# Kernel optimization log

Hardware: AMD Instinct MI355X
Metric: run time of the kernel (lower is better)

The kernel has to match this reference:

```python
import jax, jax.numpy as jnp
import numpy as np

LR = 0.1          # learning_rate
THRESHOLD = 0.1   # surprise_threshold (fixed; adaptive_threshold=False / eval path)
TEMP = 0.1        # temperature
EPS = 1e-6

B, S, DK, DV = 64, 1024, 128, 128


def setup_inputs() -> dict:
    key = jax.random.key(0)
    k1, k2 = jax.random.split(key)
    return {
        "memory": jnp.zeros((B, DV, DK), dtype=jnp.float32),
        "key": jax.random.normal(k1, (B, S, DK), dtype=jnp.float32),
        "value": jax.random.normal(k2, (B, S, DV), dtype=jnp.float32),
    }


def reference(memory, key, value):
    # memory: (B, DV, DK); key: (B, S, DK); value: (B, S, DV)
    # Sequential delta-rule fast-weight update with surprise gating.
    def step(mem, kv):
        k_t, v_t = kv                                  # (B, DK), (B, DV)
        k_n = k_t / (jnp.linalg.norm(k_t, axis=-1, keepdims=True) + EPS)
        predicted = jnp.einsum('bvk,bk->bv', mem, k_n)  # (B, DV)
        surprise = predicted - v_t                      # (B, DV)
        s_norm = jnp.linalg.norm(surprise, axis=-1, keepdims=True)  # (B, 1)
        gate = jax.nn.sigmoid((s_norm - THRESHOLD) / TEMP)          # (B, 1)
        # forget_term + lr*learn_term = (predicted + lr*surprise) outer k_n
        update = (predicted + LR * surprise)[:, :, None] * k_n[:, None, :]
        mem = mem - gate[:, :, None] * update
        return mem, gate

    # scan over the sequence axis
    kv_seq = (jnp.swapaxes(key, 0, 1), jnp.swapaxes(value, 0, 1))  # (S, B, *)
    mem_final, gates = jax.lax.scan(step, memory, kv_seq)
    gate_values = jnp.swapaxes(gates, 0, 1)  # (B, S, 1)
    return mem_final, gate_values
```

## Files before the change

### kernel.cpp

```cpp
#include <hip/hip_runtime.h>
#include <math.h>

#define B_    64
#define S_    1024
#define DK_   128
#define DV_   128
#define T_    16
#define NC_   (S_ / T_)
#define KP_   (DK_ + 4)
#define LR_   0.1f
#define LRP1_ 1.1f
#define THR_  0.1f
#define ITEMP_ 10.0f
#define EPS_  1e-6f

template<int CTRL>
__device__ __forceinline__ float dpp_add(float x) {
  int t = __builtin_amdgcn_update_dpp(0, __float_as_int(x), CTRL, 0xf, 0xf, true);
  return x + __int_as_float(t);
}
__device__ __forceinline__ float wave_sum64(float x) {
  x = dpp_add<0x111>(x); x = dpp_add<0x112>(x); x = dpp_add<0x114>(x);
  x = dpp_add<0x118>(x); x = dpp_add<0x142>(x); x = dpp_add<0x143>(x);
  return __int_as_float(__builtin_amdgcn_readlane(__float_as_int(x), 63));
}
__device__ __forceinline__ float row16_sum(float x) {
  x = dpp_add<0x111>(x); x = dpp_add<0x112>(x);
  x = dpp_add<0x114>(x); x = dpp_add<0x118>(x);
  return x;
}
__device__ __forceinline__ float rdlane(float v, int l) {
  return __int_as_float(__builtin_amdgcn_readlane(__float_as_int(v), l));
}
__device__ __forceinline__ float dot4(float4 a, float4 b) {
  return fmaf(a.x, b.x, fmaf(a.y, b.y, fmaf(a.z, b.z, a.w * b.w)));
}
__device__ __forceinline__ void gll16(const float* g, float* l) {
  __builtin_amdgcn_global_load_lds(
      (const __attribute__((address_space(1))) unsigned int*)g,
      (__attribute__((address_space(3))) unsigned int*)l, 16, 0, 0);
}

__global__ __launch_bounds__(512, 2)
void sgm_kernel(const float* __restrict__ mem_in,
                const float* __restrict__ key,
                const float* __restrict__ value,
                float* __restrict__ out) {
  const int b = blockIdx.x, tid = threadIdx.x;
  const int g = tid >> 4, h = tid & 15, lane = tid & 63, wv = tid >> 6;

  __shared__ __align__(16) float kS[2][T_][KP_];
  __shared__ __align__(16) float vS[2][T_][KP_];
  __shared__ __align__(16) float rawL[T_][DK_];
  __shared__ __align__(16) float cuL[T_][DK_];
  __shared__ __align__(16) float GT[2][T_][T_];
  __shared__ __align__(16) float gateL[S_];

  float4 mA[4], mB[4];
  {
    const float4* Mp = reinterpret_cast<const float4*>(mem_in + (size_t)b * DV_ * DK_);
    #pragma unroll
    for (int rr = 0; rr < 4; ++rr) {
      mA[rr] = Mp[(4*g + rr) * 32 + h];
      mB[rr] = Mp[(4*g + rr) * 32 + 16 + h];
    }
  }
  const float* kb = key   + (size_t)b * S_ * DK_;
  const float* vb = value + (size_t)b * S_ * DV_;

  const int pPair = (tid - 64) >> 1;
  int tP = 0, jP = 0;
  {
    int t = 0, pp = pPair;
    if (wv > 0 && pPair < 136) {
      while (pp > t) { pp -= (t + 1); ++t; }
      tP = t; jP = pp;
    }
  }

  auto stage = [&](int cc) {
    if (wv == 0 && lane < 32) {
      #pragma unroll
      for (int t = 0; t < T_; ++t)
        gll16(kb + (size_t)(cc*T_ + t)*DK_ + lane*4, &kS[cc & 1][t][0]);
    }
    if (wv == 1 && lane < 32) {
      #pragma unroll
      for (int t = 0; t < T_; ++t)
        gll16(vb + (size_t)(cc*T_ + t)*DV_ + lane*4, &vS[cc & 1][t][0]);
    }
  };

  float4 kxR[16];

  auto applyUpdate = [&](int pb) {
    #pragma unroll
    for (int j = 0; j < T_; ++j) {
      const float4* kj = reinterpret_cast<const float4*>(&kS[pb][j][0]);
      const float4 ky = kj[16 + h];
      const float4 cu = *reinterpret_cast<const float4*>(&cuL[j][4 * g]);
      const float cc4[4] = {cu.x, cu.y, cu.z, cu.w};
      #pragma unroll
      for (int rr = 0; rr < 4; ++rr) {
        mA[rr].x = fmaf(-cc4[rr], kxR[j].x, mA[rr].x);
        mA[rr].y = fmaf(-cc4[rr], kxR[j].y, mA[rr].y);
        mA[rr].z = fmaf(-cc4[rr], kxR[j].z, mA[rr].z);
        mA[rr].w = fmaf(-cc4[rr], kxR[j].w, mA[rr].w);
        mB[rr].x = fmaf(-cc4[rr], ky.x, mB[rr].x);
        mB[rr].y = fmaf(-cc4[rr], ky.y, mB[rr].y);
        mB[rr].z = fmaf(-cc4[rr], ky.z, mB[rr].z);
        mB[rr].w = fmaf(-cc4[rr], ky.w, mB[rr].w);
      }
    }
  };

  auto gramPhase = [&](int cc) {
    const int cb1 = cc & 1;
    const int h2 = tid & 1;
    if (wv > 0 && pPair < 136) {
      const float4* kj4 = reinterpret_cast<const float4*>(&kS[cb1][jP][h2*64]);
      const float4* kt4 = reinterpret_cast<const float4*>(&kS[cb1][tP][h2*64]);
      float acc = 0.f;
      #pragma unroll
      for (int i = 0; i < 16; ++i) acc += dot4(kj4[i], kt4[i]);
      int sw = __builtin_amdgcn_update_dpp(0, __float_as_int(acc), 0xB1, 0xf, 0xf, true);
      const float tot = acc + __int_as_float(sw);
      if (h2 == 0) GT[cb1][tP][jP] = tot;
    }
  };

  stage(0);
  if (wv < 2) asm volatile("s_waitcnt vmcnt(0)" ::: "memory");
  __syncthreads();
  gramPhase(0);
  asm volatile("s_waitcnt lgkmcnt(0)" ::: "memory");
  __builtin_amdgcn_s_barrier();
  asm volatile("" ::: "memory");

  for (int c = 0; c < NC_; ++c) {
    const int cb = c & 1;

    if (c > 0) applyUpdate((c - 1) & 1);

    asm volatile("s_waitcnt lgkmcnt(0)" ::: "memory");
    __builtin_amdgcn_s_barrier();
    asm volatile("" ::: "memory");
    if (c + 1 < NC_) stage(c + 1);

    #pragma unroll
    for (int t = 0; t < T_; ++t) {
      const float4* kt = reinterpret_cast<const float4*>(&kS[cb][t][0]);
      const float4 kx = kt[h];
      const float4 ky = kt[16 + h];
      kxR[t] = kx;
      float a0 = dot4(mA[0], kx) + dot4(mB[0], ky);
      float a1 = dot4(mA[1], kx) + dot4(mB[1], ky);
      float a2 = dot4(mA[2], kx) + dot4(mB[2], ky);
      float a3 = dot4(mA[3], kx) + dot4(mB[3], ky);
      a0 = row16_sum(a0); a1 = row16_sum(a1);
      a2 = row16_sum(a2); a3 = row16_sum(a3);
      if (h == 15)
        *reinterpret_cast<float4*>(&rawL[t][4 * g]) = make_float4(a0, a1, a2, a3);
    }

    if (wv < 2) asm volatile("s_waitcnt vmcnt(0)" ::: "memory");
    asm volatile("s_waitcnt lgkmcnt(0)" ::: "memory");
    __builtin_amdgcn_s_barrier();
    asm volatile("" ::: "memory");

    if (wv == 0) {
      const int sj = lane & 15;
      const float rinv = 1.0f / (sqrtf(GT[cb][sj][sj]) + EPS_);
      float cu0[T_], cu1[T_];
      #pragma unroll
      for (int t = 0; t < T_; ++t) {
        const float grt = GT[cb][t][sj];
        const float rin_t = rdlane(rinv, t);
        float y0 = 0.f, y1 = 0.f;
        #pragma unroll
        for (int j = 0; j < T_; ++j) if (j < t) {
          const float gjt = rdlane(grt, j);
          y0 = fmaf(gjt, cu0[j], y0);
          y1 = fmaf(gjt, cu1[j], y1);
        }
        const float2 rv  = *reinterpret_cast<const float2*>(&rawL[t][2*lane]);
        const float2 vvt = *reinterpret_cast<const float2*>(&vS[cb][t][2*lane]);
        const float pred0 = rin_t * (rv.x - y0);
        const float pred1 = rin_t * (rv.y - y1);
        const float s0 = pred0 - vvt.x, s1 = pred1 - vvt.y;
        const float s2 = wave_sum64(fmaf(s0, s0, s1 * s1));
        const float gg = 1.0f / (1.0f + __expf((THR_ - sqrtf(s2)) * ITEMP_));
        if (lane == 0) gateL[c*T_ + t] = gg;
        const float ct = gg * rin_t;
        const float u0 = fmaf(LRP1_, pred0, -(LR_ * vvt.x));
        const float u1 = fmaf(LRP1_, pred1, -(LR_ * vvt.y));
        cu0[t] = ct * u0; cu1[t] = ct * u1;
        *reinterpret_cast<float2*>(&cuL[t][2*lane]) = make_float2(cu0[t], cu1[t]);
      }
    } else {
      if (c + 1 < NC_) gramPhase(c + 1);
    }

    asm volatile("s_waitcnt lgkmcnt(0)" ::: "memory");
    __builtin_amdgcn_s_barrier();
    asm volatile("" ::: "memory");
  }

  applyUpdate((NC_ - 1) & 1);

  {
    float4* Op = reinterpret_cast<float4*>(out + (size_t)b * DV_ * DK_);
    #pragma unroll
    for (int rr = 0; rr < 4; ++rr) {
      Op[(4*g + rr) * 32 + h] = mA[rr];
      Op[(4*g + rr) * 32 + 16 + h] = mB[rr];
    }
    float2* Gp = reinterpret_cast<float2*>(out + (size_t)B_ * DV_ * DK_ + (size_t)b * S_);
    Gp[tid] = reinterpret_cast<const float2*>(gateL)[tid];
  }
}

extern "C" void kernel_launch(void* const* d_in, const int* in_sizes, int n_in,
                              void* d_out, int out_size, void* d_ws, size_t ws_size,
                              hipStream_t stream) {
  const float* mem = (const float*)d_in[0];
  const float* key = (const float*)d_in[1];
  const float* val = (const float*)d_in[2];
  float* out = (float*)d_out;
  sgm_kernel<<<B_, 512, 0, stream>>>(mem, key, val, out);
}
```

Baseline: 562.0 us.

## Deepen key/value staging to two chunks ahead and drop a barrier per chunk

```diff
diff --git a/kernel.cpp b/kernel.cpp
--- a/kernel.cpp
+++ b/kernel.cpp
@@ -41,7 +41,7 @@
       (__attribute__((address_space(3))) unsigned int*)l, 16, 0, 0);
 }
 
-__global__ __launch_bounds__(512, 2)
+__global__ __launch_bounds__(512, 1)
 void sgm_kernel(const float* __restrict__ mem_in,
                 const float* __restrict__ key,
                 const float* __restrict__ value,
@@ -49,8 +49,8 @@
   const int b = blockIdx.x, tid = threadIdx.x;
   const int g = tid >> 4, h = tid & 15, lane = tid & 63, wv = tid >> 6;
 
-  __shared__ __align__(16) float kS[2][T_][KP_];
-  __shared__ __align__(16) float vS[2][T_][KP_];
+  __shared__ __align__(16) float kS[4][T_][KP_];
+  __shared__ __align__(16) float vS[3][T_][KP_];
   __shared__ __align__(16) float rawL[T_][DK_];
   __shared__ __align__(16) float cuL[T_][DK_];
   __shared__ __align__(16) float GT[2][T_][T_];
@@ -72,7 +72,7 @@
   int tP = 0, jP = 0;
   {
     int t = 0, pp = pPair;
-    if (wv > 0 && pPair < 136) {
+    if (wv > 0 && pPair >= 0 && pPair < 136) {
       while (pp > t) { pp -= (t + 1); ++t; }
       tP = t; jP = pp;
     }
@@ -82,21 +82,21 @@
     if (wv == 0 && lane < 32) {
       #pragma unroll
       for (int t = 0; t < T_; ++t)
-        gll16(kb + (size_t)(cc*T_ + t)*DK_ + lane*4, &kS[cc & 1][t][0]);
+        gll16(kb + (size_t)(cc*T_ + t)*DK_ + lane*4, &kS[cc & 3][t][0]);
     }
     if (wv == 1 && lane < 32) {
       #pragma unroll
       for (int t = 0; t < T_; ++t)
-        gll16(vb + (size_t)(cc*T_ + t)*DV_ + lane*4, &vS[cc & 1][t][0]);
+        gll16(vb + (size_t)(cc*T_ + t)*DV_ + lane*4, &vS[cc % 3][t][0]);
     }
   };
 
   float4 kxR[16];
 
-  auto applyUpdate = [&](int pb) {
+  auto applyUpdate = [&](int sl) {
     #pragma unroll
     for (int j = 0; j < T_; ++j) {
-      const float4* kj = reinterpret_cast<const float4*>(&kS[pb][j][0]);
+      const float4* kj = reinterpret_cast<const float4*>(&kS[sl][j][0]);
       const float4 ky = kj[16 + h];
       const float4 cu = *reinterpret_cast<const float4*>(&cuL[j][4 * g]);
       const float cc4[4] = {cu.x, cu.y, cu.z, cu.w};
@@ -115,21 +115,24 @@
   };
 
   auto gramPhase = [&](int cc) {
-    const int cb1 = cc & 1;
+    const int sl = cc & 3, pb = cc & 1;
     const int h2 = tid & 1;
     if (wv > 0 && pPair < 136) {
-      const float4* kj4 = reinterpret_cast<const float4*>(&kS[cb1][jP][h2*64]);
-      const float4* kt4 = reinterpret_cast<const float4*>(&kS[cb1][tP][h2*64]);
+      const float4* kj4 = reinterpret_cast<const float4*>(&kS[sl][jP][h2*64]);
+      const float4* kt4 = reinterpret_cast<const float4*>(&kS[sl][tP][h2*64]);
       float acc = 0.f;
       #pragma unroll
-      for (int i = 0; i < 16; ++i) acc += dot4(kj4[i], kt4[i]);
+      for (int i = 0; i < 16; ++i) {
+        const int ii = (i + pPair) & 15;
+        acc += dot4(kj4[ii], kt4[ii]);
+      }
       int sw = __builtin_amdgcn_update_dpp(0, __float_as_int(acc), 0xB1, 0xf, 0xf, true);
       const float tot = acc + __int_as_float(sw);
-      if (h2 == 0) GT[cb1][tP][jP] = tot;
+      if (h2 == 0) GT[pb][tP][jP] = tot;
     }
   };
 
-  stage(0);
+  stage(0); stage(1);
   if (wv < 2) asm volatile("s_waitcnt vmcnt(0)" ::: "memory");
   __syncthreads();
   gramPhase(0);
@@ -139,17 +142,15 @@
 
   for (int c = 0; c < NC_; ++c) {
     const int cb = c & 1;
-
-    if (c > 0) applyUpdate((c - 1) & 1);
-
-    asm volatile("s_waitcnt lgkmcnt(0)" ::: "memory");
-    __builtin_amdgcn_s_barrier();
-    asm volatile("" ::: "memory");
-    if (c + 1 < NC_) stage(c + 1);
+    const bool staged = (c + 2 < NC_);
+
+    if (staged) stage(c + 2);
+
+    if (c > 0) applyUpdate((c - 1) & 3);
 
     #pragma unroll
     for (int t = 0; t < T_; ++t) {
-      const float4* kt = reinterpret_cast<const float4*>(&kS[cb][t][0]);
+      const float4* kt = reinterpret_cast<const float4*>(&kS[c & 3][t][0]);
       const float4 kx = kt[h];
       const float4 ky = kt[16 + h];
       kxR[t] = kx;
@@ -163,7 +164,10 @@
         *reinterpret_cast<float4*>(&rawL[t][4 * g]) = make_float4(a0, a1, a2, a3);
     }
 
-    if (wv < 2) asm volatile("s_waitcnt vmcnt(0)" ::: "memory");
+    if (wv < 2) {
+      if (staged) asm volatile("s_waitcnt vmcnt(16)" ::: "memory");
+      else        asm volatile("s_waitcnt vmcnt(0)"  ::: "memory");
+    }
     asm volatile("s_waitcnt lgkmcnt(0)" ::: "memory");
     __builtin_amdgcn_s_barrier();
     asm volatile("" ::: "memory");
@@ -184,7 +188,7 @@
           y1 = fmaf(gjt, cu1[j], y1);
         }
         const float2 rv  = *reinterpret_cast<const float2*>(&rawL[t][2*lane]);
-        const float2 vvt = *reinterpret_cast<const float2*>(&vS[cb][t][2*lane]);
+        const float2 vvt = *reinterpret_cast<const float2*>(&vS[c % 3][t][2*lane]);
         const float pred0 = rin_t * (rv.x - y0);
         const float pred1 = rin_t * (rv.y - y1);
         const float s0 = pred0 - vvt.x, s1 = pred1 - vvt.y;
@@ -206,7 +210,7 @@
     asm volatile("" ::: "memory");
   }
 
-  applyUpdate((NC_ - 1) & 1);
+  applyUpdate((NC_ - 1) & 3);
 
   {
     float4* Op = reinterpret_cast<float4*>(out + (size_t)b * DV_ * DK_);
```

Result: faster. 543.2 us, median of 2 (-3.3%).
